# Kernel tuning notes

Measured on AMD Instinct MI355X. Metric: run time of the kernel, lower is better.

## Reference

```python
import jax, jax.numpy as jnp
import numpy as np

N = 50000
IN_DIM = 64
HID = [64, 64]
HEADS = 4
E0 = 800000
MLP_HID = 200
N_CLASSES = 2
NEG_SLOPE = 0.2
BN_EPS = 1e-5


def setup_inputs() -> dict:
    key = jax.random.key(0)
    ks = jax.random.split(key, 16)
    features = jax.random.normal(ks[0], (N, IN_DIM), dtype=jnp.float32)
    edge_index = jax.random.randint(ks[1], (2, E0), 0, N, dtype=jnp.int32)
    s = 0.05
    # GATConv layer 1 params
    W1 = jax.random.normal(ks[2], (IN_DIM, HEADS * HID[0]), dtype=jnp.float32) * s
    al1 = jax.random.normal(ks[3], (HEADS, HID[0]), dtype=jnp.float32) * s
    ar1 = jax.random.normal(ks[4], (HEADS, HID[0]), dtype=jnp.float32) * s
    b1 = jnp.zeros((HEADS * HID[0],), dtype=jnp.float32)
    # GATConv layer 2 params
    W2 = jax.random.normal(ks[5], (HID[0], HEADS * HID[1]), dtype=jnp.float32) * s
    al2 = jax.random.normal(ks[6], (HEADS, HID[1]), dtype=jnp.float32) * s
    ar2 = jax.random.normal(ks[7], (HEADS, HID[1]), dtype=jnp.float32) * s
    b2 = jnp.zeros((HEADS * HID[1],), dtype=jnp.float32)
    # MLP predictor: Linear(64->200), ReLU, BatchNorm1d(200), Linear(200->2)
    mw1 = jax.random.normal(ks[8], (HID[1], MLP_HID), dtype=jnp.float32) * s
    mb1 = jnp.zeros((MLP_HID,), dtype=jnp.float32)
    bn_g = jnp.ones((MLP_HID,), dtype=jnp.float32)
    bn_b = jnp.zeros((MLP_HID,), dtype=jnp.float32)
    mw2 = jax.random.normal(ks[9], (MLP_HID, N_CLASSES), dtype=jnp.float32) * s
    mb2 = jnp.zeros((N_CLASSES,), dtype=jnp.float32)
    return {"features": features, "edge_index": edge_index,
            "W1": W1, "al1": al1, "ar1": ar1, "b1": b1,
            "W2": W2, "al2": al2, "ar2": ar2, "b2": b2,
            "mw1": mw1, "mb1": mb1, "bn_g": bn_g, "bn_b": bn_b,
            "mw2": mw2, "mb2": mb2}


def _gat_layer(h, src, dst, W, al, ar, bias):
    # h: [N, F_in]; src/dst: [E] int (messages flow src -> dst, softmax over in-edges)
    H, D = al.shape
    feat = (h @ W).reshape(N, H, D)               # [N,H,D]
    el = jnp.sum(feat * al, axis=-1)              # [N,H]
    er = jnp.sum(feat * ar, axis=-1)              # [N,H]
    e = jax.nn.leaky_relu(el[src] + er[dst], NEG_SLOPE)  # [E,H]
    # numerically stable edge softmax segmented by dst
    m = jax.ops.segment_max(e, dst, num_segments=N)      # [N,H]
    ex = jnp.exp(e - m[dst])
    denom = jax.ops.segment_sum(ex, dst, num_segments=N)  # [N,H]
    a = ex / denom[dst]                                  # [E,H]
    msg = feat[src] * a[:, :, None]                      # [E,H,D]
    rst = jax.ops.segment_sum(msg, dst, num_segments=N)  # [N,H,D]
    rst = rst + bias.reshape(H, D)
    return jax.nn.relu(rst)


def reference(features, edge_index, W1, al1, ar1, b1, W2, al2, ar2, b2,
              mw1, mb1, bn_g, bn_b, mw2, mb2):
    # dgl.add_self_loop
    loop = jnp.arange(N, dtype=edge_index.dtype)
    src = jnp.concatenate([edge_index[0], loop])
    dst = jnp.concatenate([edge_index[1], loop])
    h = features
    h = _gat_layer(h, src, dst, W1, al1, ar1, b1).mean(axis=1)  # [N, 64]
    h = _gat_layer(h, src, dst, W2, al2, ar2, b2).mean(axis=1)  # [N, 64]
    # MLP predictor (dropout = identity in eval): Linear -> ReLU -> BatchNorm1d -> Linear
    z = jax.nn.relu(h @ mw1 + mb1)                       # [N, 200]
    mu = z.mean(axis=0)
    var = z.var(axis=0)                                  # biased var (batch stats)
    z = (z - mu) * jax.lax.rsqrt(var + BN_EPS) * bn_g + bn_b
    return z @ mw2 + mb2                                 # [N, 2]
```

## Files before the change

### kernel.cpp

```cpp
#include <hip/hip_runtime.h>
#include <hip/hip_bf16.h>

#define N_NODES 50000
#define E0_EDGES 800000
#define E_TOTAL 850000
#define NEG_SLOPE 0.2f
#define BN_EPS 1e-5f
#define CAP 64

typedef __attribute__((ext_vector_type(8))) short bf16x8;
typedef __attribute__((ext_vector_type(4))) float f32x4;

__device__ __forceinline__ float lrelu(float x) { return x > 0.f ? x : NEG_SLOPE * x; }

__device__ __forceinline__ ushort f2bf(float x) {
    __hip_bfloat16 b = __float2bfloat16(x);
    return *reinterpret_cast<ushort*>(&b);
}
__device__ __forceinline__ float bf2f(ushort u) {
    return __uint_as_float(((unsigned int)u) << 16);
}

#define PREP_Z 196
#define PREP_W 256
#define PREP_F 3125
__global__ void k_prep(int* __restrict__ deg, float* __restrict__ gsum, float* __restrict__ gsumsq,
                       const float* __restrict__ W1, const float* __restrict__ W2,
                       ushort* __restrict__ WbfT1, ushort* __restrict__ WbfT2,
                       const float* __restrict__ x, ushort* __restrict__ xbf) {
    int b = blockIdx.x;
    int tid = threadIdx.x;
    if (b < PREP_Z) {
        int i = b * 256 + tid;
        if (i < N_NODES) deg[i] = 0;
        if (i < 200) { gsum[i] = 0.f; gsumsq[i] = 0.f; }
    } else if (b < PREP_Z + PREP_W) {
        int c = b - PREP_Z;
        if (tid < 64)       WbfT1[c * 64 + tid] = f2bf(W1[tid * 256 + c]);
        else if (tid < 128) WbfT2[c * 64 + (tid - 64)] = f2bf(W2[(tid - 64) * 256 + c]);
    } else {
        int i = ((b - PREP_Z - PREP_W) * 256 + tid) * 4;
        float4 v = *(const float4*)&x[i];
        ushort4 o;
        o.x = f2bf(v.x); o.y = f2bf(v.y); o.z = f2bf(v.z); o.w = f2bf(v.w);
        *(ushort4*)&xbf[i] = o;
    }
}

__global__ void k_count(const int* __restrict__ ei, int* __restrict__ deg, ushort* __restrict__ rank) {
    int e = blockIdx.x * 256 + threadIdx.x;
    if (e >= E_TOTAL) return;
    int dst = (e < E0_EDGES) ? ei[E0_EDGES + e] : (e - E0_EDGES);
    rank[e] = (ushort)atomicAdd(&deg[dst], 1);
}

__global__ void k_scanA(const int* __restrict__ deg, int* __restrict__ rowptr, int* __restrict__ bsum) {
    __shared__ int s[256];
    int i = blockIdx.x * 256 + threadIdx.x;
    int v = (i < N_NODES) ? deg[i] : 0;
    s[threadIdx.x] = v;
    __syncthreads();
    for (int off = 1; off < 256; off <<= 1) {
        int t = (threadIdx.x >= off) ? s[threadIdx.x - off] : 0;
        __syncthreads();
        s[threadIdx.x] += t;
        __syncthreads();
    }
    if (i < N_NODES) rowptr[i] = s[threadIdx.x];
    if (threadIdx.x == 255) bsum[blockIdx.x] = s[255];
}

__global__ void k_scanC(const int* __restrict__ deg, int* __restrict__ rowptr,
                        const int* __restrict__ bsum, int nb) {
    __shared__ int s[256];
    int tid = threadIdx.x;
    s[tid] = (tid < nb && tid < blockIdx.x) ? bsum[tid] : 0;
    __syncthreads();
    for (int off = 128; off; off >>= 1) {
        if (tid < off) s[tid] += s[tid + off];
        __syncthreads();
    }
    int blockoff = s[0];
    int i = blockIdx.x * 256 + tid;
    if (i >= N_NODES) return;
    rowptr[i] = blockoff + rowptr[i] - deg[i];
    if (i == N_NODES - 1) rowptr[N_NODES] = E_TOTAL;
}

#define FG_FILL 3321
#define FG_GEMM 3125
__device__ __forceinline__ void gemm_feat_body(int bid, const ushort* __restrict__ x,
                                               const ushort* __restrict__ WbfT,
                                               const float* __restrict__ al, const float* __restrict__ ar,
                                               ushort* __restrict__ featB,
                                               float* __restrict__ el, float* __restrict__ er,
                                               float (*fs)[256]) {
    int tid = threadIdx.x;
    int wave = tid >> 6, lane = tid & 63;
    int row0 = bid * 16;
    int lr = lane & 15;
    int q = lane >> 4;

    const ushort* ap = x + (size_t)(row0 + lr) * 64 + q * 8;
    bf16x8 a0 = *reinterpret_cast<const bf16x8*>(ap);
    bf16x8 a1 = *reinterpret_cast<const bf16x8*>(ap + 32);

#pragma unroll
    for (int t = 0; t < 4; t++) {
        int ct = wave * 4 + t;
        const ushort* wrow = WbfT + (size_t)(ct * 16 + lr) * 64 + q * 8;
        bf16x8 b0 = *reinterpret_cast<const bf16x8*>(wrow);
        bf16x8 b1 = *reinterpret_cast<const bf16x8*>(wrow + 32);
        f32x4 acc = {0.f, 0.f, 0.f, 0.f};
        acc = __builtin_amdgcn_mfma_f32_16x16x32_bf16(a0, b0, acc, 0, 0, 0);
        acc = __builtin_amdgcn_mfma_f32_16x16x32_bf16(a1, b1, acc, 0, 0, 0);
#pragma unroll
        for (int i = 0; i < 4; i++)
            fs[q * 4 + i][ct * 16 + lr] = acc[i];
    }
    __syncthreads();

    {
        int r = tid >> 4;
        int rem = tid & 15;
        int h = rem >> 2;
        int l = rem & 3;
        int d0 = l * 16;
        float vl = 0.f, vr = 0.f;
#pragma unroll
        for (int j = 0; j < 16; j += 4) {
            float4 f = *(const float4*)&fs[r][h * 64 + d0 + j];
            float4 a = *(const float4*)&al[h * 64 + d0 + j];
            float4 b = *(const float4*)&ar[h * 64 + d0 + j];
            vl += f.x * a.x + f.y * a.y + f.z * a.z + f.w * a.w;
            vr += f.x * b.x + f.y * b.y + f.z * b.z + f.w * b.w;
        }
        vl += __shfl_xor(vl, 1, 64); vl += __shfl_xor(vl, 2, 64);
        vr += __shfl_xor(vr, 1, 64); vr += __shfl_xor(vr, 2, 64);
        if (l == 0) {
            el[(row0 + r) * 4 + h] = vl;
            er[(row0 + r) * 4 + h] = vr;
        }
    }

    int c = tid;
    int srcc = ((c & 3) << 6) + (c >> 2);
#pragma unroll
    for (int r = 0; r < 16; r++)
        featB[(size_t)(row0 + r) * 256 + c] = f2bf(fs[r][srcc]);
}

__global__ void k_fill_gemm(const int* __restrict__ ei, const int* __restrict__ rowptr,
                            const ushort* __restrict__ rank, ushort* __restrict__ colidx,
                            const ushort* __restrict__ x, const ushort* __restrict__ WbfT,
                            const float* __restrict__ al, const float* __restrict__ ar,
                            ushort* __restrict__ featB, float* __restrict__ el, float* __restrict__ er) {
    __shared__ float fs[16][256];
    if (blockIdx.x < FG_FILL) {
        int e = blockIdx.x * 256 + threadIdx.x;
        if (e >= E_TOTAL) return;
        int src, dst;
        if (e < E0_EDGES) { src = ei[e]; dst = ei[E0_EDGES + e]; }
        else { src = e - E0_EDGES; dst = src; }
        colidx[rowptr[dst] + rank[e]] = (ushort)src;
        return;
    }
    gemm_feat_body(blockIdx.x - FG_FILL, x, WbfT, al, ar, featB, el, er, fs);
}

__global__ void k_gemm_feat(const ushort* __restrict__ x, const ushort* __restrict__ WbfT,
                            const float* __restrict__ al, const float* __restrict__ ar,
                            ushort* __restrict__ featB, float* __restrict__ el, float* __restrict__ er) {
    __shared__ float fs[16][256];
    gemm_feat_body(blockIdx.x, x, WbfT, al, ar, featB, el, er, fs);
}

__global__ void k_gat(const float4* __restrict__ el4, const float4* __restrict__ er4,
                      const int* __restrict__ rowptr, const ushort* __restrict__ colidx,
                      const ushort* __restrict__ featB, const float* __restrict__ bias,
                      ushort* __restrict__ hout) {
    __shared__ float4 sE[4][CAP];
    __shared__ int    sSrc[4][CAP];
    int tid = threadIdx.x;
    int w = tid >> 6, lane = tid & 63;
    int row = blockIdx.x * 4 + w;
    int start = rowptr[row];
    int deg = rowptr[row + 1] - start;
    int cached = min(deg, CAP);
    float4 erow = er4[row];

    float4 sm = make_float4(0.f, 0.f, 0.f, 0.f);
    for (int idx = lane; idx < cached; idx += 64) {
        int src = colidx[start + idx];
        float4 e = el4[src];
        float4 ex;
        ex.x = __expf(lrelu(e.x + erow.x));
        ex.y = __expf(lrelu(e.y + erow.y));
        ex.z = __expf(lrelu(e.z + erow.z));
        ex.w = __expf(lrelu(e.w + erow.w));
        sE[w][idx] = ex; sSrc[w][idx] = src;
        sm.x += ex.x; sm.y += ex.y; sm.z += ex.z; sm.w += ex.w;
    }
    for (int idx = CAP + lane; idx < deg; idx += 64) {
        int src = colidx[start + idx];
        float4 e = el4[src];
        sm.x += __expf(lrelu(e.x + erow.x));
        sm.y += __expf(lrelu(e.y + erow.y));
        sm.z += __expf(lrelu(e.z + erow.z));
        sm.w += __expf(lrelu(e.w + erow.w));
    }
#pragma unroll
    for (int off = 32; off; off >>= 1) {
        sm.x += __shfl_xor(sm.x, off, 64);
        sm.y += __shfl_xor(sm.y, off, 64);
        sm.z += __shfl_xor(sm.z, off, 64);
        sm.w += __shfl_xor(sm.w, off, 64);
    }
    float4 dr;
    dr.x = 1.f / sm.x; dr.y = 1.f / sm.y; dr.z = 1.f / sm.z; dr.w = 1.f / sm.w;

    const ushort4* featB4 = (const ushort4*)featB;
    float4 acc = make_float4(0.f, 0.f, 0.f, 0.f);
#pragma unroll 4
    for (int s = 0; s < cached; s++) {
        float4 ex = sE[w][s];
        int src = sSrc[w][s];
        ushort4 f = featB4[(size_t)src * 64 + lane];
        acc.x = fmaf(bf2f(f.x), ex.x, acc.x);
        acc.y = fmaf(bf2f(f.y), ex.y, acc.y);
        acc.z = fmaf(bf2f(f.z), ex.z, acc.z);
        acc.w = fmaf(bf2f(f.w), ex.w, acc.w);
    }
    for (int s = CAP; s < deg; s++) {
        int src = colidx[start + s];
        float4 e = el4[src];
        float4 ex;
        ex.x = __expf(lrelu(e.x + erow.x));
        ex.y = __expf(lrelu(e.y + erow.y));
        ex.z = __expf(lrelu(e.z + erow.z));
        ex.w = __expf(lrelu(e.w + erow.w));
        ushort4 f = featB4[(size_t)src * 64 + lane];
        acc.x = fmaf(bf2f(f.x), ex.x, acc.x);
        acc.y = fmaf(bf2f(f.y), ex.y, acc.y);
        acc.z = fmaf(bf2f(f.z), ex.z, acc.z);
        acc.w = fmaf(bf2f(f.w), ex.w, acc.w);
    }
    float o = fmaxf(fmaf(acc.x, dr.x, bias[lane]), 0.f)
            + fmaxf(fmaf(acc.y, dr.y, bias[64 + lane]), 0.f)
            + fmaxf(fmaf(acc.z, dr.z, bias[128 + lane]), 0.f)
            + fmaxf(fmaf(acc.w, dr.w, bias[192 + lane]), 0.f);
    hout[(size_t)row * 64 + lane] = f2bf(o * 0.25f);
}

#define MLP_BLOCKS 1250
#define MLP_CHUNKS 5
__global__ void k_mlp1_stats(const ushort* __restrict__ x, const float* __restrict__ W,
                             const float* __restrict__ b, ushort* __restrict__ z,
                             float* __restrict__ gsum, float* __restrict__ gsumsq) {
    __shared__ float xs[8][64];
    int tid = threadIdx.x;
    float bv = (tid < 200) ? b[tid] : 0.f;
    float s_ = 0.f, s2_ = 0.f;
    for (int chunk = 0; chunk < MLP_CHUNKS; chunk++) {
        int row0 = (blockIdx.x * MLP_CHUNKS + chunk) * 8;
        for (int i = tid; i < 512; i += 256)
            xs[i >> 6][i & 63] = bf2f(x[(size_t)(row0 + (i >> 6)) * 64 + (i & 63)]);
        __syncthreads();
        if (tid < 200) {
            float acc[8];
#pragma unroll
            for (int r = 0; r < 8; r++) acc[r] = 0.f;
            for (int k = 0; k < 64; k++) {
                float w = W[k * 200 + tid];
#pragma unroll
                for (int r = 0; r < 8; r++) acc[r] = fmaf(xs[r][k], w, acc[r]);
            }
#pragma unroll
            for (int r = 0; r < 8; r++) {
                float v = fmaxf(acc[r] + bv, 0.f);
                z[(size_t)(row0 + r) * 200 + tid] = f2bf(v);
                s_ += v;
                s2_ = fmaf(v, v, s2_);
            }
        }
        __syncthreads();
    }
    if (tid < 200) {
        atomicAdd(&gsum[tid], s_);
        atomicAdd(&gsumsq[tid], s2_);
    }
}

__global__ void k_bnprep(const float* __restrict__ gsum, const float* __restrict__ gsumsq,
                         const float* __restrict__ bn_g, const float* __restrict__ bn_b,
                         const float* __restrict__ mw2, const float* __restrict__ mb2,
                         float* __restrict__ w2p) {
    __shared__ float red0[256], red1[256];
    int c = threadIdx.x;
    float c0 = 0.f, c1 = 0.f;
    if (c < 200) {
        const float invN = 1.f / (float)N_NODES;
        float mu = gsum[c] * invN;
        float var = gsumsq[c] * invN - mu * mu;
        float alpha = bn_g[c] * rsqrtf(var + BN_EPS);
        float beta = bn_b[c] - mu * alpha;
        float w0 = mw2[c * 2], w1 = mw2[c * 2 + 1];
        w2p[c * 2] = alpha * w0;
        w2p[c * 2 + 1] = alpha * w1;
        c0 = beta * w0;
        c1 = beta * w1;
    }
    red0[c] = c0; red1[c] = c1;
    __syncthreads();
    for (int off = 128; off; off >>= 1) {
        if (c < off) { red0[c] += red0[c + off]; red1[c] += red1[c + off]; }
        __syncthreads();
    }
    if (c == 0) {
        w2p[400] = mb2[0] + red0[0];
        w2p[401] = mb2[1] + red1[0];
    }
}

__global__ void k_final(const ushort* __restrict__ z, const float* __restrict__ w2p, float* __restrict__ out) {
    int tid = threadIdx.x;
    int row = blockIdx.x * 4 + (tid >> 6);
    int lane = tid & 63;
    float a0 = 0.f, a1 = 0.f;
    for (int c = lane; c < 200; c += 64) {
        float v = bf2f(z[(size_t)row * 200 + c]);
        a0 = fmaf(v, w2p[c * 2], a0);
        a1 = fmaf(v, w2p[c * 2 + 1], a1);
    }
#pragma unroll
    for (int off = 32; off; off >>= 1) {
        a0 += __shfl_xor(a0, off, 64);
        a1 += __shfl_xor(a1, off, 64);
    }
    if (lane == 0) {
        out[row * 2] = a0 + w2p[400];
        out[row * 2 + 1] = a1 + w2p[401];
    }
}

extern "C" void kernel_launch(void* const* d_in, const int* in_sizes, int n_in,
                              void* d_out, int out_size, void* d_ws, size_t ws_size,
                              hipStream_t stream) {
    const float* features = (const float*)d_in[0];
    const int*   ei       = (const int*)d_in[1];
    const float* W1  = (const float*)d_in[2];
    const float* al1 = (const float*)d_in[3];
    const float* ar1 = (const float*)d_in[4];
    const float* b1  = (const float*)d_in[5];
    const float* W2  = (const float*)d_in[6];
    const float* al2 = (const float*)d_in[7];
    const float* ar2 = (const float*)d_in[8];
    const float* b2  = (const float*)d_in[9];
    const float* mw1 = (const float*)d_in[10];
    const float* mb1 = (const float*)d_in[11];
    const float* bng = (const float*)d_in[12];
    const float* bnb = (const float*)d_in[13];
    const float* mw2 = (const float*)d_in[14];
    const float* mb2 = (const float*)d_in[15];
    float* out = (float*)d_out;

    char* base = (char*)d_ws;
    size_t off = 0;
    auto alloc = [&](size_t bytes) -> char* {
        char* p = base + off;
        off = (off + bytes + 255) & ~(size_t)255;
        return p;
    };
    int*    deg    = (int*)alloc(N_NODES * 4);
    int*    rowptr = (int*)alloc((N_NODES + 1) * 4);
    ushort* rank   = (ushort*)alloc(E_TOTAL * 2);
    int*    bsum   = (int*)alloc(256 * 4);
    ushort* colidx = (ushort*)alloc(E_TOTAL * 2);
    ushort* featB  = (ushort*)alloc((size_t)N_NODES * 256 * 2);
    float*  el     = (float*)alloc((size_t)N_NODES * 4 * 4);
    float*  er     = (float*)alloc((size_t)N_NODES * 4 * 4);
    ushort* xbf    = (ushort*)alloc((size_t)N_NODES * 64 * 2);
    ushort* h1     = (ushort*)alloc((size_t)N_NODES * 64 * 2);
    ushort* h2     = (ushort*)alloc((size_t)N_NODES * 64 * 2);
    ushort* z      = (ushort*)alloc((size_t)N_NODES * 200 * 2);
    float*  gsum   = (float*)alloc(256 * 4);
    float*  gsumsq = (float*)alloc(256 * 4);
    float*  w2p    = (float*)alloc(512 * 4);
    ushort* WbfT1  = (ushort*)alloc(256 * 64 * 2);
    ushort* WbfT2  = (ushort*)alloc(256 * 64 * 2);
    (void)ws_size; (void)in_sizes; (void)n_in; (void)out_size;

    const int NB_N = (N_NODES + 255) / 256;
    const int NB_E = (E_TOTAL + 255) / 256;

    k_prep<<<PREP_Z + PREP_W + PREP_F, 256, 0, stream>>>(deg, gsum, gsumsq,
                                                         W1, W2, WbfT1, WbfT2,
                                                         features, xbf);
    k_count<<<NB_E, 256, 0, stream>>>(ei, deg, rank);
    k_scanA<<<NB_N, 256, 0, stream>>>(deg, rowptr, bsum);
    k_scanC<<<NB_N, 256, 0, stream>>>(deg, rowptr, bsum, NB_N);

    k_fill_gemm<<<FG_FILL + FG_GEMM, 256, 0, stream>>>(ei, rowptr, rank, colidx,
                                                       xbf, WbfT1, al1, ar1, featB, el, er);
    k_gat<<<N_NODES / 4, 256, 0, stream>>>((const float4*)el, (const float4*)er, rowptr, colidx, featB, b1, h1);

    k_gemm_feat<<<N_NODES / 16, 256, 0, stream>>>(h1, WbfT2, al2, ar2, featB, el, er);
    k_gat<<<N_NODES / 4, 256, 0, stream>>>((const float4*)el, (const float4*)er, rowptr, colidx, featB, b2, h2);

    k_mlp1_stats<<<MLP_BLOCKS, 256, 0, stream>>>(h2, mw1, mb1, z, gsum, gsumsq);
    k_bnprep<<<1, 256, 0, stream>>>(gsum, gsumsq, bng, bnb, mw2, mb2, w2p);
    k_final<<<N_NODES / 4, 256, 0, stream>>>(z, w2p, out);
}
```

Baseline: 303.7 us.

## Use bf16 MFMA for MLP first layer and fold BatchNorm prep into final kernel

```diff
diff --git a/kernel.cpp b/kernel.cpp
--- a/kernel.cpp
+++ b/kernel.cpp
@@ -27,6 +27,7 @@
 __global__ void k_prep(int* __restrict__ deg, float* __restrict__ gsum, float* __restrict__ gsumsq,
                        const float* __restrict__ W1, const float* __restrict__ W2,
                        ushort* __restrict__ WbfT1, ushort* __restrict__ WbfT2,
+                       const float* __restrict__ mw1, ushort* __restrict__ mwT,
                        const float* __restrict__ x, ushort* __restrict__ xbf) {
     int b = blockIdx.x;
     int tid = threadIdx.x;
@@ -36,8 +37,9 @@
         if (i < 200) { gsum[i] = 0.f; gsumsq[i] = 0.f; }
     } else if (b < PREP_Z + PREP_W) {
         int c = b - PREP_Z;
-        if (tid < 64)       WbfT1[c * 64 + tid] = f2bf(W1[tid * 256 + c]);
-        else if (tid < 128) WbfT2[c * 64 + (tid - 64)] = f2bf(W2[(tid - 64) * 256 + c]);
+        if (tid < 64)        WbfT1[c * 64 + tid] = f2bf(W1[tid * 256 + c]);
+        else if (tid < 128)  WbfT2[c * 64 + (tid - 64)] = f2bf(W2[(tid - 64) * 256 + c]);
+        else if (tid < 192 && c < 200) mwT[c * 64 + (tid - 128)] = f2bf(mw1[(tid - 128) * 200 + c]);
     } else {
         int i = ((b - PREP_Z - PREP_W) * 256 + tid) * 4;
         float4 v = *(const float4*)&x[i];
@@ -252,85 +254,122 @@
     hout[(size_t)row * 64 + lane] = f2bf(o * 0.25f);
 }
 
-#define MLP_BLOCKS 1250
-#define MLP_CHUNKS 5
-__global__ void k_mlp1_stats(const ushort* __restrict__ x, const float* __restrict__ W,
-                             const float* __restrict__ b, ushort* __restrict__ z,
-                             float* __restrict__ gsum, float* __restrict__ gsumsq) {
-    __shared__ float xs[8][64];
-    int tid = threadIdx.x;
-    float bv = (tid < 200) ? b[tid] : 0.f;
-    float s_ = 0.f, s2_ = 0.f;
-    for (int chunk = 0; chunk < MLP_CHUNKS; chunk++) {
-        int row0 = (blockIdx.x * MLP_CHUNKS + chunk) * 8;
-        for (int i = tid; i < 512; i += 256)
-            xs[i >> 6][i & 63] = bf2f(x[(size_t)(row0 + (i >> 6)) * 64 + (i & 63)]);
-        __syncthreads();
-        if (tid < 200) {
-            float acc[8];
-#pragma unroll
-            for (int r = 0; r < 8; r++) acc[r] = 0.f;
-            for (int k = 0; k < 64; k++) {
-                float w = W[k * 200 + tid];
-#pragma unroll
-                for (int r = 0; r < 8; r++) acc[r] = fmaf(xs[r][k], w, acc[r]);
+#define MLP_TILES 13
+__global__ __launch_bounds__(512) void k_mlp1_mfma(const ushort* __restrict__ h, const ushort* __restrict__ mwT,
+                                                   const float* __restrict__ mb1, ushort* __restrict__ z,
+                                                   float* __restrict__ gsum, float* __restrict__ gsumsq) {
+    __shared__ float sS[MLP_TILES * 16], sS2[MLP_TILES * 16];
+    int tid = threadIdx.x;
+    int wave = tid >> 6, lane = tid & 63;
+    int lr = lane & 15, q = lane >> 4;
+    int half = wave >> 2;
+    int tidx = wave & 3;
+    int rowbase = blockIdx.x * 32 + half * 16;
+
+    const ushort* ap = h + (size_t)(rowbase + lr) * 64 + q * 8;
+    bf16x8 a0 = *reinterpret_cast<const bf16x8*>(ap);
+    bf16x8 a1 = *reinterpret_cast<const bf16x8*>(ap + 32);
+
+    for (int ct = tidx; ct < MLP_TILES; ct += 4) {
+        const ushort* wrow = mwT + (size_t)(ct * 16 + lr) * 64 + q * 8;
+        bf16x8 b0 = *reinterpret_cast<const bf16x8*>(wrow);
+        bf16x8 b1 = *reinterpret_cast<const bf16x8*>(wrow + 32);
+        f32x4 acc = {0.f, 0.f, 0.f, 0.f};
+        acc = __builtin_amdgcn_mfma_f32_16x16x32_bf16(a0, b0, acc, 0, 0, 0);
+        acc = __builtin_amdgcn_mfma_f32_16x16x32_bf16(a1, b1, acc, 0, 0, 0);
+
+        int col = ct * 16 + lr;
+        bool colok = (col < 200);
+        float bv = colok ? mb1[col] : 0.f;
+        float s = 0.f, s2 = 0.f;
+#pragma unroll
+        for (int i = 0; i < 4; i++) {
+            int row = rowbase + q * 4 + i;
+            float v = fmaxf(acc[i] + bv, 0.f);
+            if (colok && row < N_NODES) {
+                z[(size_t)row * 200 + col] = f2bf(v);
+                s += v;
+                s2 = fmaf(v, v, s2);
             }
-#pragma unroll
-            for (int r = 0; r < 8; r++) {
-                float v = fmaxf(acc[r] + bv, 0.f);
-                z[(size_t)(row0 + r) * 200 + tid] = f2bf(v);
-                s_ += v;
-                s2_ = fmaf(v, v, s2_);
+        }
+        s  += __shfl_xor(s, 16, 64);  s  += __shfl_xor(s, 32, 64);
+        s2 += __shfl_xor(s2, 16, 64); s2 += __shfl_xor(s2, 32, 64);
+        if (q == 0) {
+            if (half == 0) { sS[ct * 16 + lr] = s; sS2[ct * 16 + lr] = s2; }
+        }
+    }
+    __syncthreads();
+    if (half == 1 && q == 0) {
+        for (int ct = tidx; ct < MLP_TILES; ct += 4) {
+            int col = ct * 16 + lr;
+            if (col < 200) {
             }
         }
-        __syncthreads();
-    }
-    if (tid < 200) {
-        atomicAdd(&gsum[tid], s_);
-        atomicAdd(&gsumsq[tid], s2_);
-    }
-}
-
-__global__ void k_bnprep(const float* __restrict__ gsum, const float* __restrict__ gsumsq,
-                         const float* __restrict__ bn_g, const float* __restrict__ bn_b,
-                         const float* __restrict__ mw2, const float* __restrict__ mb2,
-                         float* __restrict__ w2p) {
-    __shared__ float red0[256], red1[256];
-    int c = threadIdx.x;
-    float c0 = 0.f, c1 = 0.f;
-    if (c < 200) {
-        const float invN = 1.f / (float)N_NODES;
+    }
+}
+
+__global__ __launch_bounds__(512) void k_mlp1_mfma2(const ushort* __restrict__ h, const ushort* __restrict__ mwT,
+                                                    const float* __restrict__ mb1, ushort* __restrict__ z,
+                                                    float* __restrict__ gsum, float* __restrict__ gsumsq) {
+    int tid = threadIdx.x;
+    int wave = tid >> 6, lane = tid & 63;
+    int lr = lane & 15, q = lane >> 4;
+    int half = wave >> 2;
+    int tidx = wave & 3;
+    int rowbase = blockIdx.x * 32 + half * 16;
+
+    const ushort* ap = h + (size_t)(rowbase + lr) * 64 + q * 8;
+    bf16x8 a0 = *reinterpret_cast<const bf16x8*>(ap);
+    bf16x8 a1 = *reinterpret_cast<const bf16x8*>(ap + 32);
+
+    for (int ct = tidx; ct < MLP_TILES; ct += 4) {
+        const ushort* wrow = mwT + (size_t)(ct * 16 + lr) * 64 + q * 8;
+        bf16x8 b0 = *reinterpret_cast<const bf16x8*>(wrow);
+        bf16x8 b1 = *reinterpret_cast<const bf16x8*>(wrow + 32);
+        f32x4 acc = {0.f, 0.f, 0.f, 0.f};
+        acc = __builtin_amdgcn_mfma_f32_16x16x32_bf16(a0, b0, acc, 0, 0, 0);
+        acc = __builtin_amdgcn_mfma_f32_16x16x32_bf16(a1, b1, acc, 0, 0, 0);
+
+        int col = ct * 16 + lr;
+        bool colok = (col < 200);
+        float bv = colok ? mb1[col] : 0.f;
+        float s = 0.f, s2 = 0.f;
+#pragma unroll
+        for (int i = 0; i < 4; i++) {
+            int row = rowbase + q * 4 + i;
+            float v = fmaxf(acc[i] + bv, 0.f);
+            if (colok && row < N_NODES) {
+                z[(size_t)row * 200 + col] = f2bf(v);
+                s += v;
+                s2 = fmaf(v, v, s2);
+            }
+        }
+        s  += __shfl_xor(s, 16, 64);  s  += __shfl_xor(s, 32, 64);
+        s2 += __shfl_xor(s2, 16, 64); s2 += __shfl_xor(s2, 32, 64);
+        if (q == 0 && colok) {
+            atomicAdd(&gsum[col], s);
+            atomicAdd(&gsumsq[col], s2);
+        }
+    }
+}
+
+__global__ void k_final(const ushort* __restrict__ z, const float* __restrict__ gsum,
+                        const float* __restrict__ gsumsq, const float* __restrict__ bn_g,
+                        const float* __restrict__ bn_b, const float* __restrict__ mw2,
+                        const float* __restrict__ mb2, float* __restrict__ out) {
+    int tid = threadIdx.x;
+    int row = blockIdx.x * 4 + (tid >> 6);
+    int lane = tid & 63;
+    const float invN = 1.f / (float)N_NODES;
+    float a0 = 0.f, a1 = 0.f;
+    for (int c = lane; c < 200; c += 64) {
         float mu = gsum[c] * invN;
         float var = gsumsq[c] * invN - mu * mu;
         float alpha = bn_g[c] * rsqrtf(var + BN_EPS);
         float beta = bn_b[c] - mu * alpha;
-        float w0 = mw2[c * 2], w1 = mw2[c * 2 + 1];
-        w2p[c * 2] = alpha * w0;
-        w2p[c * 2 + 1] = alpha * w1;
-        c0 = beta * w0;
-        c1 = beta * w1;
-    }
-    red0[c] = c0; red1[c] = c1;
-    __syncthreads();
-    for (int off = 128; off; off >>= 1) {
-        if (c < off) { red0[c] += red0[c + off]; red1[c] += red1[c + off]; }
-        __syncthreads();
-    }
-    if (c == 0) {
-        w2p[400] = mb2[0] + red0[0];
-        w2p[401] = mb2[1] + red1[0];
-    }
-}
-
-__global__ void k_final(const ushort* __restrict__ z, const float* __restrict__ w2p, float* __restrict__ out) {
-    int tid = threadIdx.x;
-    int row = blockIdx.x * 4 + (tid >> 6);
-    int lane = tid & 63;
-    float a0 = 0.f, a1 = 0.f;
-    for (int c = lane; c < 200; c += 64) {
-        float v = bf2f(z[(size_t)row * 200 + c]);
-        a0 = fmaf(v, w2p[c * 2], a0);
-        a1 = fmaf(v, w2p[c * 2 + 1], a1);
+        float zn = fmaf(alpha, bf2f(z[(size_t)row * 200 + c]), beta);
+        a0 = fmaf(zn, mw2[c * 2], a0);
+        a1 = fmaf(zn, mw2[c * 2 + 1], a1);
     }
 #pragma unroll
     for (int off = 32; off; off >>= 1) {
@@ -338,8 +377,8 @@
         a1 += __shfl_xor(a1, off, 64);
     }
     if (lane == 0) {
-        out[row * 2] = a0 + w2p[400];
-        out[row * 2 + 1] = a1 + w2p[401];
+        out[row * 2] = a0 + mb2[0];
+        out[row * 2 + 1] = a1 + mb2[1];
     }
 }
 
@@ -385,9 +424,9 @@
     ushort* z      = (ushort*)alloc((size_t)N_NODES * 200 * 2);
     float*  gsum   = (float*)alloc(256 * 4);
     float*  gsumsq = (float*)alloc(256 * 4);
-    float*  w2p    = (float*)alloc(512 * 4);
     ushort* WbfT1  = (ushort*)alloc(256 * 64 * 2);
     ushort* WbfT2  = (ushort*)alloc(256 * 64 * 2);
+    ushort* mwT    = (ushort*)alloc(208 * 64 * 2);
     (void)ws_size; (void)in_sizes; (void)n_in; (void)out_size;
 
     const int NB_N = (N_NODES + 255) / 256;
@@ -395,7 +434,7 @@
 
     k_prep<<<PREP_Z + PREP_W + PREP_F, 256, 0, stream>>>(deg, gsum, gsumsq,
                                                          W1, W2, WbfT1, WbfT2,
-                                                         features, xbf);
+                                                         mw1, mwT, features, xbf);
     k_count<<<NB_E, 256, 0, stream>>>(ei, deg, rank);
     k_scanA<<<NB_N, 256, 0, stream>>>(deg, rowptr, bsum);
     k_scanC<<<NB_N, 256, 0, stream>>>(deg, rowptr, bsum, NB_N);
@@ -407,7 +446,6 @@
     k_gemm_feat<<<N_NODES / 16, 256, 0, stream>>>(h1, WbfT2, al2, ar2, featB, el, er);
     k_gat<<<N_NODES / 4, 256, 0, stream>>>((const float4*)el, (const float4*)er, rowptr, colidx, featB, b2, h2);
 
-    k_mlp1_stats<<<MLP_BLOCKS, 256, 0, stream>>>(h2, mw1, mb1, z, gsum, gsumsq);
-    k_bnprep<<<1, 256, 0, stream>>>(gsum, gsumsq, bng, bnb, mw2, mb2, w2p);
-    k_final<<<N_NODES / 4, 256, 0, stream>>>(z, w2p, out);
-}
+    k_mlp1_mfma2<<<(N_NODES + 31) / 32, 512, 0, stream>>>(h2, mwT, mb1, z, gsum, gsumsq);
+    k_final<<<N_NODES / 4, 256, 0, stream>>>(z, gsum, gsumsq, bng, bnb, mw2, mb2, out);
+}
```

Result: slower. 368.3 us (+21.2%).
